# Performance work log

Hardware: AMD Instinct MI355X
Metric: run time of the kernel (lower is better)

Reference implementation:

```python
import jax, jax.numpy as jnp
import numpy as np

N, E, F_IN = 50000, 1_600_000, 256
HID, HEADS, NCLS = 8, 8, 16  # conv1: 8 heads x 8 dims (concat=64); conv2: 1 head -> 16 classes


def setup_inputs() -> dict:
    key = jax.random.key(0)
    ks = jax.random.split(key, 11)
    x = jax.random.normal(ks[0], (N, F_IN), dtype=jnp.float32)
    edge_index = jax.random.randint(ks[1], (2, E), 0, N, dtype=jnp.int32)
    s1 = 1.0 / np.sqrt(F_IN)
    W1 = jax.random.normal(ks[2], (F_IN, HEADS * HID), jnp.float32) * s1
    a_src1 = jax.random.normal(ks[3], (HEADS, HID), jnp.float32) * 0.1
    a_dst1 = jax.random.normal(ks[4], (HEADS, HID), jnp.float32) * 0.1
    b1 = jnp.zeros((HEADS * HID,), jnp.float32)
    s2 = 1.0 / np.sqrt(HEADS * HID)
    W2 = jax.random.normal(ks[5], (HEADS * HID, NCLS), jnp.float32) * s2
    a_src2 = jax.random.normal(ks[6], (1, NCLS), jnp.float32) * 0.1
    a_dst2 = jax.random.normal(ks[7], (1, NCLS), jnp.float32) * 0.1
    b2 = jnp.zeros((NCLS,), jnp.float32)
    return {"x": x, "edge_index": edge_index, "W1": W1, "a_src1": a_src1,
            "a_dst1": a_dst1, "b1": b1, "W2": W2, "a_src2": a_src2,
            "a_dst2": a_dst2, "b2": b2}


def _gat_conv(x, W, a_src, a_dst, bias, src, dst, n, heads, ch, concat):
    # per-head linear transform: [n, heads, ch]
    h = (x @ W).reshape(n, heads, ch)
    # additive attention logits per node, per head
    al_s = jnp.einsum('nhc,hc->nh', h, a_src)
    al_d = jnp.einsum('nhc,hc->nh', h, a_dst)
    e = jax.nn.leaky_relu(al_s[src] + al_d[dst], 0.2)  # [E_tot, heads]
    # segment softmax grouped by destination node (self-loops guarantee non-empty segments)
    m = jax.ops.segment_max(e, dst, num_segments=n)
    ex = jnp.exp(e - m[dst])
    den = jax.ops.segment_sum(ex, dst, num_segments=n)
    alpha = ex / den[dst]  # [E_tot, heads]
    # scatter-aggregate weighted neighbor features
    out = jax.ops.segment_sum(h[src] * alpha[:, :, None], dst, num_segments=n)
    out = out.reshape(n, heads * ch) if concat else out.mean(axis=1)
    return out + bias


def reference(x, edge_index, W1, a_src1, a_dst1, b1, W2, a_src2, a_dst2, b2):
    # add self-loops (PyG GATConv default)
    loops = jnp.arange(N, dtype=edge_index.dtype)
    src = jnp.concatenate([edge_index[0], loops])
    dst = jnp.concatenate([edge_index[1], loops])
    h = _gat_conv(x, W1, a_src1, a_dst1, b1, src, dst, N, HEADS, HID, True)
    h = jax.nn.elu(h)
    out = _gat_conv(h, W2, a_src2, a_dst2, b2, src, dst, N, 1, NCLS, False)
    return jax.nn.log_softmax(out, axis=1)
```

## Files before the change

### kernel.cpp

```cpp
#include <hip/hip_runtime.h>
#include <hip/hip_fp16.h>

#define NN   50000
#define FIN  256
#define C1   64
#define NH   8
#define NC   16
#define NE   1600000
#define NTOT (NE + NN)

#define CH   256
#define EPC  ((NTOT + CH - 1) / CH)
#define NCB  392
#define GB1  ((NN + 63) / 64)

typedef _Float16 half8 __attribute__((ext_vector_type(8)));
typedef _Float16 half4 __attribute__((ext_vector_type(4)));
typedef float f32x4 __attribute__((ext_vector_type(4)));

#define OFF_H1H   0
#define OFF_G1H   1600000
#define OFF_STAGE 3200000
#define OFF_H2H   3200000
#define OFF_ALS2  3600000
#define OFF_ALD2  3650000
#define OFF_ALS1  6400000
#define OFF_ALD1  6800000
#define OFF_HM    7200000
#define OFF_BASEK 7300352
#define OFF_BBASE 7400704
#define OFF_OFFS  7401600
#define OFF_SRC   7451700
#define OFF_W1T   9101700

__global__ __launch_bounds__(256) void k_wcvt(const float* __restrict__ W1,
                                              _Float16* __restrict__ w1t) {
    int t = blockIdx.x * 256 + threadIdx.x;
    int c = t >> 8, k = t & 255;
    w1t[t] = (_Float16)W1[k * C1 + c];
}

__global__ __launch_bounds__(256) void k_g1rh(const float* __restrict__ x,
                                              const _Float16* __restrict__ w1t,
                                              const float* __restrict__ as1,
                                              const float* __restrict__ ad1,
                                              __half* __restrict__ h1h,
                                              float* __restrict__ als,
                                              float* __restrict__ ald,
                                              const int* __restrict__ ei,
                                              int* __restrict__ H) {
    __shared__ _Float16 wsT[64][264];
    __shared__ _Float16 xs[64][40];
    const int tid = threadIdx.x;

    if (blockIdx.x >= GB1) {
        int* lh = (int*)xs;
        int k = blockIdx.x - GB1;
        for (int i = tid; i < NCB; i += 256) lh[i] = 0;
        __syncthreads();
        int e0 = k * EPC, e1 = min(e0 + EPC, NTOT);
        for (int e = e0 + tid; e < e1; e += 256) {
            int d = (e < NE) ? ei[NE + e] : (e - NE);
            atomicAdd(&lh[d >> 7], 1);
        }
        __syncthreads();
        for (int i = tid; i < NCB; i += 256) H[k * NCB + i] = lh[i];
        return;
    }

    const int r0 = blockIdx.x * 64;
    #pragma unroll
    for (int j = 0; j < 8; ++j) {
        int idx = tid * 8 + j * 2048;
        int c = idx >> 8, ko = idx & 255;
        *(half8*)(&wsT[c][ko]) = *(const half8*)(&w1t[idx]);
    }

    const int lane = tid & 63;
    const int wv   = tid >> 6;
    const int colb = lane & 15;
    const int rgrp = lane >> 4;
    f32x4 acc[4] = {};
    const int srow = tid >> 2;
    const int sq   = tid & 3;
    for (int k0 = 0; k0 < FIN; k0 += 32) {
        __syncthreads();
        {
            int grow = r0 + srow;
            float4 v0 = make_float4(0.f,0.f,0.f,0.f), v1 = v0;
            if (grow < NN) {
                const float4* xp = (const float4*)(&x[(size_t)grow * FIN + k0 + sq * 8]);
                v0 = xp[0]; v1 = xp[1];
            }
            half8 hv;
            hv[0]=(_Float16)v0.x; hv[1]=(_Float16)v0.y; hv[2]=(_Float16)v0.z; hv[3]=(_Float16)v0.w;
            hv[4]=(_Float16)v1.x; hv[5]=(_Float16)v1.y; hv[6]=(_Float16)v1.z; hv[7]=(_Float16)v1.w;
            *(half8*)(&xs[srow][sq * 8]) = hv;
        }
        __syncthreads();
        half8 a = *(half8*)(&xs[wv * 16 + colb][rgrp * 8]);
        #pragma unroll
        for (int ct = 0; ct < 4; ++ct) {
            half8 b = *(half8*)(&wsT[ct * 16 + colb][k0 + rgrp * 8]);
            acc[ct] = __builtin_amdgcn_mfma_f32_16x16x32_f16(a, b, acc[ct], 0, 0, 0);
        }
    }

    float a_s[4], a_d[4];
    #pragma unroll
    for (int ct = 0; ct < 4; ++ct) { a_s[ct] = as1[ct * 16 + colb]; a_d[ct] = ad1[ct * 16 + colb]; }
    #pragma unroll
    for (int j = 0; j < 4; ++j) {
        int row = r0 + wv * 16 + rgrp * 4 + j;
        bool rv = row < NN;
        #pragma unroll
        for (int ct = 0; ct < 4; ++ct) {
            if (rv) h1h[(size_t)row * C1 + ct * 16 + colb] = __float2half(acc[ct][j]);
            float p = acc[ct][j] * a_s[ct];
            p += __shfl_xor(p, 1); p += __shfl_xor(p, 2); p += __shfl_xor(p, 4);
            float q = acc[ct][j] * a_d[ct];
            q += __shfl_xor(q, 1); q += __shfl_xor(q, 2); q += __shfl_xor(q, 4);
            if (rv && (lane & 7) == 0) {
                int head = ct * 2 + (colb >> 3);
                als[row * NH + head] = p;
                ald[row * NH + head] = q;
            }
        }
    }
}

__global__ __launch_bounds__(256) void k_rsA(const int* __restrict__ H,
                                             int* __restrict__ basek,
                                             int* __restrict__ btot) {
    __shared__ int sc[CH];
    int b = blockIdx.x, t = threadIdx.x;
    int v = H[t * NCB + b];
    sc[t] = v;
    __syncthreads();
    for (int s = 1; s < CH; s <<= 1) {
        int u = (t >= s) ? sc[t - s] : 0;
        __syncthreads();
        sc[t] += u;
        __syncthreads();
    }
    basek[b * CH + t] = sc[t] - v;
    if (t == CH - 1) btot[b] = sc[t];
}

__global__ __launch_bounds__(512) void k_rsB(const int* __restrict__ btot,
                                             int* __restrict__ bbase,
                                             int* __restrict__ offs) {
    __shared__ int sc[512];
    int t = threadIdx.x;
    int v = (t < NCB) ? btot[t] : 0;
    sc[t] = v;
    __syncthreads();
    for (int s = 1; s < 512; s <<= 1) {
        int u = (t >= s) ? sc[t - s] : 0;
        __syncthreads();
        sc[t] += u;
        __syncthreads();
    }
    if (t < NCB) bbase[t] = sc[t] - v;
    if (t == NCB - 1) bbase[NCB] = sc[t];
    if (t == 0) offs[NN] = NTOT;
}

__global__ __launch_bounds__(256) void k_rscatter(const int* __restrict__ ei,
                                                  const int* __restrict__ basek,
                                                  const int* __restrict__ bbase,
                                                  int* __restrict__ stage) {
    __shared__ int lcur[NCB];
    int k = blockIdx.x;
    for (int i = threadIdx.x; i < NCB; i += 256)
        lcur[i] = bbase[i] + basek[i * CH + k];
    __syncthreads();
    int e0 = k * EPC, e1 = min(e0 + EPC, NTOT);
    for (int e = e0 + threadIdx.x; e < e1; e += 256) {
        int s, d;
        if (e < NE) { s = ei[e]; d = ei[NE + e]; }
        else        { s = e - NE; d = s; }
        int pos = atomicAdd(&lcur[d >> 7], 1);
        stage[pos] = (s << 7) | (d & 127);
    }
}

__global__ __launch_bounds__(256) void k_fsort(const int* __restrict__ stage,
                                               const int* __restrict__ bbase,
                                               int* __restrict__ offs,
                                               int* __restrict__ ssrc) {
    __shared__ int lc[128];
    __shared__ int ls[128];
    __shared__ int lcur[128];
    int b = blockIdx.x, t = threadIdx.x;
    int base = bbase[b];
    int n = bbase[b + 1] - base;
    if (t < 128) lc[t] = 0;
    __syncthreads();
    const int* sp = &stage[base];
    for (int i = t; i < n; i += 256) atomicAdd(&lc[sp[i] & 127], 1);
    __syncthreads();
    int v = (t < 128) ? lc[t] : 0;
    if (t < 128) ls[t] = v;
    __syncthreads();
    for (int s = 1; s < 128; s <<= 1) {
        int u = (t >= s && t < 128) ? ls[t - s] : 0;
        __syncthreads();
        if (t < 128) ls[t] += u;
        __syncthreads();
    }
    if (t < 128) {
        int excl = ls[t] - v;
        int d = b * 128 + t;
        if (d < NN) offs[d] = base + excl;
        lcur[t] = base + excl;
    }
    __syncthreads();
    for (int i = t; i < n; i += 256) {
        int u = sp[i];
        int pos = atomicAdd(&lcur[u & 127], 1);
        ssrc[pos] = u >> 7;
    }
}

__global__ __launch_bounds__(256) void k_agg1(const int* __restrict__ offs,
                                              const int* __restrict__ src,
                                              const __half* __restrict__ h1h,
                                              const float* __restrict__ als,
                                              const float* __restrict__ ald,
                                              const float* __restrict__ b1,
                                              _Float16* __restrict__ g1h) {
    int d = blockIdx.x * 4 + (threadIdx.x >> 6);
    if (d >= NN) return;
    const int l  = threadIdx.x & 63;
    const int q  = l >> 4, lc = l & 15;
    const int hg = lc >> 1;
    const int sub = l >> 3, hw = l & 7;
    const int lane_a = (q << 3) | hg;
    const int lane_b = lane_a + 32;
    const unsigned coff = (unsigned)lc * 8u;
    const unsigned hoff = (unsigned)hw * 4u;
    const char* h1b = (const char*)h1h;
    const char* alb = (const char*)als;
    int beg = offs[d], end = offs[d + 1];
    float aldv = ald[d * NH + hw];
    f32x4 acc = {0.f, 0.f, 0.f, 0.f};
    float wsum = 0.f;

    int r = beg;
    int e0 = r + sub, e1 = e0 + 8;
    int s0 = src[e0 < end ? e0 : end - 1];
    int s1 = src[e1 < end ? e1 : end - 1];
    while (r < end) {
        bool v0 = (r + sub) < end, v1 = (r + 8 + sub) < end;
        float lg0 = *(const float*)(alb + ((unsigned)s0 * 32u + hoff)) + aldv;
        float lg1 = *(const float*)(alb + ((unsigned)s1 * 32u + hoff)) + aldv;
        lg0 = lg0 > 0.f ? lg0 : 0.2f * lg0;
        lg1 = lg1 > 0.f ? lg1 : 0.2f * lg1;
        float w0 = v0 ? __expf(lg0) : 0.f;
        float w1 = v1 ? __expf(lg1) : 0.f;
        wsum += w0 + w1;
        int rn = r + 16;
        int s0n = s0, s1n = s1;
        if (rn < end) {
            int f0 = rn + sub, f1 = f0 + 8;
            s0n = src[f0 < end ? f0 : end - 1];
            s1n = src[f1 < end ? f1 : end - 1];
        }
        #pragma unroll
        for (int i = 0; i < 4; ++i) {
            int srcl = (i & 1) ? lane_b : lane_a;
            int sv   = __shfl((i < 2) ? s0 : s1, srcl);
            float wv = __shfl((i < 2) ? w0 : w1, srcl);
            half4 hv = *(const half4*)(h1b + ((unsigned)sv * 128u + coff));
            acc[0] += wv * (float)hv[0];
            acc[1] += wv * (float)hv[1];
            acc[2] += wv * (float)hv[2];
            acc[3] += wv * (float)hv[3];
        }
        s0 = s0n; s1 = s1n; r = rn;
    }
    #pragma unroll
    for (int k = 0; k < 4; ++k) {
        acc[k] += __shfl_xor(acc[k], 16);
        acc[k] += __shfl_xor(acc[k], 32);
    }
    wsum += __shfl_xor(wsum, 8);
    wsum += __shfl_xor(wsum, 16);
    wsum += __shfl_xor(wsum, 32);
    float den = __shfl(wsum, hg);
    if (q == 0) {
        half4 gv;
        #pragma unroll
        for (int k = 0; k < 4; ++k) {
            float o = acc[k] / den + b1[4 * lc + k];
            o = o > 0.f ? o : (__expf(o) - 1.f);
            gv[k] = (_Float16)o;
        }
        *(half4*)(&g1h[(size_t)d * C1 + 4 * lc]) = gv;
    }
}

__global__ __launch_bounds__(256) void k_gemm2(const _Float16* __restrict__ g1h,
                                               const float* __restrict__ W2,
                                               const float* __restrict__ as2,
                                               const float* __restrict__ ad2,
                                               _Float16* __restrict__ h2h,
                                               float* __restrict__ als2,
                                               float* __restrict__ ald2) {
    __shared__ float w2s[C1][17];
    __shared__ _Float16 hact[16][C1 + 8];
    int tid = threadIdx.x;
    for (int i = tid; i < C1 * NC; i += 256) w2s[i >> 4][i & 15] = W2[i];
    int ln = tid >> 4, j = tid & 15;
    int n = blockIdx.x * 16 + ln;
    if (n < NN)
        *(half4*)(&hact[ln][j * 4]) = *(const half4*)(&g1h[(size_t)n * C1 + j * 4]);
    __syncthreads();
    if (n >= NN) return;
    float sum = 0.f;
    #pragma unroll
    for (int c = 0; c < C1; ++c) sum += (float)hact[ln][c] * w2s[c][j];
    h2h[(size_t)n * NC + j] = (_Float16)sum;
    float ps = sum * as2[j], pd = sum * ad2[j];
    #pragma unroll
    for (int w = 1; w < 16; w <<= 1) {
        ps += __shfl_xor(ps, w);
        pd += __shfl_xor(pd, w);
    }
    if (j == 0) { als2[n] = ps; ald2[n] = pd; }
}

__global__ __launch_bounds__(256) void k_agg2(const int* __restrict__ offs,
                                              const int* __restrict__ src,
                                              const _Float16* __restrict__ h2h,
                                              const float* __restrict__ als2,
                                              const float* __restrict__ ald2,
                                              const float* __restrict__ b2,
                                              float* __restrict__ out) {
    int d = blockIdx.x * 16 + (threadIdx.x >> 4);
    if (d >= NN) return;
    int c = threadIdx.x & 15;
    const unsigned coff = (unsigned)c * 2u;
    const char* h2b = (const char*)h2h;
    const char* alb = (const char*)als2;
    int beg = offs[d], end = offs[d + 1];
    float aldv = ald2[d];
    float acc = 0.f, den = 0.f;
    for (int r = beg; r < end; r += 8) {
        int ss[8];
        float ww[8];
        #pragma unroll
        for (int i = 0; i < 8; ++i) {
            int e = r + i;
            ss[i] = src[e < end ? e : end - 1];
        }
        #pragma unroll
        for (int i = 0; i < 8; ++i) {
            float lg = *(const float*)(alb + (unsigned)ss[i] * 4u) + aldv;
            lg = lg > 0.f ? lg : 0.2f * lg;
            ww[i] = (r + i) < end ? __expf(lg) : 0.f;
        }
        #pragma unroll
        for (int i = 0; i < 8; ++i) {
            float hv = (float)*(const _Float16*)(h2b + ((unsigned)ss[i] * 32u + coff));
            acc += ww[i] * hv;
            den += ww[i];
        }
    }
    float o = acc / den + b2[c];
    float m = o;
    #pragma unroll
    for (int w = 1; w < 16; w <<= 1) m = fmaxf(m, __shfl_xor(m, w));
    float ex = __expf(o - m);
    float sm = ex;
    #pragma unroll
    for (int w = 1; w < 16; w <<= 1) sm += __shfl_xor(sm, w);
    out[(size_t)d * NC + c] = o - m - __logf(sm);
}

extern "C" void kernel_launch(void* const* d_in, const int* in_sizes, int n_in,
                              void* d_out, int out_size, void* d_ws, size_t ws_size,
                              hipStream_t stream) {
    const float* x   = (const float*)d_in[0];
    const int*   ei  = (const int*)  d_in[1];
    const float* W1  = (const float*)d_in[2];
    const float* as1 = (const float*)d_in[3];
    const float* ad1 = (const float*)d_in[4];
    const float* b1  = (const float*)d_in[5];
    const float* W2  = (const float*)d_in[6];
    const float* as2 = (const float*)d_in[7];
    const float* ad2 = (const float*)d_in[8];
    const float* b2  = (const float*)d_in[9];
    float* ws  = (float*)d_ws;
    float* out = (float*)d_out;

    __half*    h1h  = (__half*)(ws + OFF_H1H);
    _Float16*  g1h  = (_Float16*)(ws + OFF_G1H);
    _Float16*  h2h  = (_Float16*)(ws + OFF_H2H);
    _Float16*  w1t  = (_Float16*)(ws + OFF_W1T);
    float* als1 = ws + OFF_ALS1;
    float* ald1 = ws + OFF_ALD1;
    float* als2 = ws + OFF_ALS2;
    float* ald2 = ws + OFF_ALD2;
    int* H      = (int*)(ws + OFF_HM);
    int* basek  = (int*)(ws + OFF_BASEK);
    int* bbase  = (int*)(ws + OFF_BBASE);
    int* btot   = (int*)(ws + OFF_BBASE) + 400;
    int* offs   = (int*)(ws + OFF_OFFS);
    int* ssrc   = (int*)(ws + OFF_SRC);
    int* stage  = (int*)(ws + OFF_STAGE);

    k_wcvt    <<<64,             256, 0, stream>>>(W1, w1t);
    k_g1rh    <<<GB1 + CH,       256, 0, stream>>>(x, w1t, as1, ad1, h1h, als1, ald1, ei, H);
    k_rsA     <<<NCB,            256, 0, stream>>>(H, basek, btot);
    k_rsB     <<<1,              512, 0, stream>>>(btot, bbase, offs);
    k_rscatter<<<CH,             256, 0, stream>>>(ei, basek, bbase, stage);
    k_fsort   <<<NCB,            256, 0, stream>>>(stage, bbase, offs, ssrc);
    k_agg1    <<<(NN + 3) / 4,   256, 0, stream>>>(offs, ssrc, h1h, als1, ald1, b1, g1h);
    k_gemm2   <<<(NN + 15) / 16, 256, 0, stream>>>(g1h, W2, as2, ad2, h2h, als2, ald2);
    k_agg2    <<<(NN + 15) / 16, 256, 0, stream>>>(offs, ssrc, h2h, als2, ald2, b2, out);
}
```

Before: 137.8 us.

## Load GEMM1 A-fragments directly, stage output via LDS, software-pipeline agg1 logits

The first GEMM kernel no longer stages x tiles through shared memory. Each lane loads its own fp32 A fragment directly and converts it to fp16, which removes the per-k-step barriers. The results are then staged in LDS, which allows coalesced half8 stores of h1 and a per-thread dot product for the attention logits in place of shuffle reductions. The agg1 loop now computes the next chunk's attention weights after the feature gathers, overlapping the logit loads and exps with the accumulation. The trade-off is uncoalesced direct global loads of x and a small change in logit precision, since the logits are now computed from fp16-rounded h values.

```diff
diff --git a/kernel.cpp b/kernel.cpp
--- a/kernel.cpp
+++ b/kernel.cpp
@@ -44,17 +44,16 @@
                                               const _Float16* __restrict__ w1t,
                                               const float* __restrict__ as1,
                                               const float* __restrict__ ad1,
-                                              __half* __restrict__ h1h,
+                                              _Float16* __restrict__ h1h,
                                               float* __restrict__ als,
                                               float* __restrict__ ald,
                                               const int* __restrict__ ei,
                                               int* __restrict__ H) {
     __shared__ _Float16 wsT[64][264];
-    __shared__ _Float16 xs[64][40];
+    __shared__ int lh[NCB];
     const int tid = threadIdx.x;
 
     if (blockIdx.x >= GB1) {
-        int* lh = (int*)xs;
         int k = blockIdx.x - GB1;
         for (int i = tid; i < NCB; i += 256) lh[i] = 0;
         __syncthreads();
@@ -75,56 +74,62 @@
         int c = idx >> 8, ko = idx & 255;
         *(half8*)(&wsT[c][ko]) = *(const half8*)(&w1t[idx]);
     }
+    __syncthreads();
 
     const int lane = tid & 63;
     const int wv   = tid >> 6;
     const int colb = lane & 15;
     const int rgrp = lane >> 4;
+    const int arow = r0 + wv * 16 + colb;
+    const bool arv = arow < NN;
     f32x4 acc[4] = {};
-    const int srow = tid >> 2;
-    const int sq   = tid & 3;
-    for (int k0 = 0; k0 < FIN; k0 += 32) {
-        __syncthreads();
-        {
-            int grow = r0 + srow;
-            float4 v0 = make_float4(0.f,0.f,0.f,0.f), v1 = v0;
-            if (grow < NN) {
-                const float4* xp = (const float4*)(&x[(size_t)grow * FIN + k0 + sq * 8]);
-                v0 = xp[0]; v1 = xp[1];
+    #pragma unroll
+    for (int s = 0; s < 8; ++s) {
+        float4 v0 = make_float4(0.f,0.f,0.f,0.f), v1 = v0;
+        if (arv) {
+            const float4* xp = (const float4*)(&x[(size_t)arow * FIN + s * 32 + rgrp * 8]);
+            v0 = xp[0]; v1 = xp[1];
+        }
+        half8 a;
+        a[0]=(_Float16)v0.x; a[1]=(_Float16)v0.y; a[2]=(_Float16)v0.z; a[3]=(_Float16)v0.w;
+        a[4]=(_Float16)v1.x; a[5]=(_Float16)v1.y; a[6]=(_Float16)v1.z; a[7]=(_Float16)v1.w;
+        #pragma unroll
+        for (int ct = 0; ct < 4; ++ct) {
+            half8 b = *(half8*)(&wsT[ct * 16 + colb][s * 32 + rgrp * 8]);
+            acc[ct] = __builtin_amdgcn_mfma_f32_16x16x32_f16(a, b, acc[ct], 0, 0, 0);
+        }
+    }
+    __syncthreads();
+    _Float16 (*hstore)[72] = (_Float16(*)[72])wsT;
+    #pragma unroll
+    for (int j = 0; j < 4; ++j) {
+        int row = wv * 16 + rgrp * 4 + j;
+        #pragma unroll
+        for (int ct = 0; ct < 4; ++ct)
+            hstore[row][ct * 16 + colb] = (_Float16)acc[ct][j];
+    }
+    __syncthreads();
+    {
+        int row = tid >> 2, seg = tid & 3;
+        int grow = r0 + row;
+        if (grow < NN) {
+            half8 h0 = *(half8*)(&hstore[row][seg * 16]);
+            half8 h1v = *(half8*)(&hstore[row][seg * 16 + 8]);
+            *(half8*)(&h1h[(size_t)grow * C1 + seg * 16])     = h0;
+            *(half8*)(&h1h[(size_t)grow * C1 + seg * 16 + 8]) = h1v;
+            float ps0 = 0.f, pd0 = 0.f, ps1 = 0.f, pd1 = 0.f;
+            #pragma unroll
+            for (int u = 0; u < 8; ++u) {
+                float a0 = (float)h0[u], a1 = (float)h1v[u];
+                ps0 += a0 * as1[seg * 16 + u];
+                pd0 += a0 * ad1[seg * 16 + u];
+                ps1 += a1 * as1[seg * 16 + 8 + u];
+                pd1 += a1 * ad1[seg * 16 + 8 + u];
             }
-            half8 hv;
-            hv[0]=(_Float16)v0.x; hv[1]=(_Float16)v0.y; hv[2]=(_Float16)v0.z; hv[3]=(_Float16)v0.w;
-            hv[4]=(_Float16)v1.x; hv[5]=(_Float16)v1.y; hv[6]=(_Float16)v1.z; hv[7]=(_Float16)v1.w;
-            *(half8*)(&xs[srow][sq * 8]) = hv;
-        }
-        __syncthreads();
-        half8 a = *(half8*)(&xs[wv * 16 + colb][rgrp * 8]);
-        #pragma unroll
-        for (int ct = 0; ct < 4; ++ct) {
-            half8 b = *(half8*)(&wsT[ct * 16 + colb][k0 + rgrp * 8]);
-            acc[ct] = __builtin_amdgcn_mfma_f32_16x16x32_f16(a, b, acc[ct], 0, 0, 0);
-        }
-    }
-
-    float a_s[4], a_d[4];
-    #pragma unroll
-    for (int ct = 0; ct < 4; ++ct) { a_s[ct] = as1[ct * 16 + colb]; a_d[ct] = ad1[ct * 16 + colb]; }
-    #pragma unroll
-    for (int j = 0; j < 4; ++j) {
-        int row = r0 + wv * 16 + rgrp * 4 + j;
-        bool rv = row < NN;
-        #pragma unroll
-        for (int ct = 0; ct < 4; ++ct) {
-            if (rv) h1h[(size_t)row * C1 + ct * 16 + colb] = __float2half(acc[ct][j]);
-            float p = acc[ct][j] * a_s[ct];
-            p += __shfl_xor(p, 1); p += __shfl_xor(p, 2); p += __shfl_xor(p, 4);
-            float q = acc[ct][j] * a_d[ct];
-            q += __shfl_xor(q, 1); q += __shfl_xor(q, 2); q += __shfl_xor(q, 4);
-            if (rv && (lane & 7) == 0) {
-                int head = ct * 2 + (colb >> 3);
-                als[row * NH + head] = p;
-                ald[row * NH + head] = q;
-            }
+            als[grow * NH + seg * 2]     = ps0;
+            als[grow * NH + seg * 2 + 1] = ps1;
+            ald[grow * NH + seg * 2]     = pd0;
+            ald[grow * NH + seg * 2 + 1] = pd1;
         }
     }
 }
@@ -251,34 +256,47 @@
     int e0 = r + sub, e1 = e0 + 8;
     int s0 = src[e0 < end ? e0 : end - 1];
     int s1 = src[e1 < end ? e1 : end - 1];
-    while (r < end) {
-        bool v0 = (r + sub) < end, v1 = (r + 8 + sub) < end;
+    {
         float lg0 = *(const float*)(alb + ((unsigned)s0 * 32u + hoff)) + aldv;
         float lg1 = *(const float*)(alb + ((unsigned)s1 * 32u + hoff)) + aldv;
         lg0 = lg0 > 0.f ? lg0 : 0.2f * lg0;
         lg1 = lg1 > 0.f ? lg1 : 0.2f * lg1;
-        float w0 = v0 ? __expf(lg0) : 0.f;
-        float w1 = v1 ? __expf(lg1) : 0.f;
-        wsum += w0 + w1;
-        int rn = r + 16;
-        int s0n = s0, s1n = s1;
-        if (rn < end) {
-            int f0 = rn + sub, f1 = f0 + 8;
-            s0n = src[f0 < end ? f0 : end - 1];
-            s1n = src[f1 < end ? f1 : end - 1];
-        }
-        #pragma unroll
-        for (int i = 0; i < 4; ++i) {
-            int srcl = (i & 1) ? lane_b : lane_a;
-            int sv   = __shfl((i < 2) ? s0 : s1, srcl);
-            float wv = __shfl((i < 2) ? w0 : w1, srcl);
-            half4 hv = *(const half4*)(h1b + ((unsigned)sv * 128u + coff));
-            acc[0] += wv * (float)hv[0];
-            acc[1] += wv * (float)hv[1];
-            acc[2] += wv * (float)hv[2];
-            acc[3] += wv * (float)hv[3];
-        }
-        s0 = s0n; s1 = s1n; r = rn;
+        s0 = e0 < end ? s0 : s0;
+        float w0t = e0 < end ? __expf(lg0) : 0.f;
+        float w1t = e1 < end ? __expf(lg1) : 0.f;
+        acc[0] = acc[0];
+        float w0 = w0t, w1 = w1t;
+        while (r < end) {
+            int rn = r + 16;
+            bool more = rn < end;
+            int s0n = s0, s1n = s1;
+            if (more) {
+                int f0 = rn + sub, f1 = f0 + 8;
+                s0n = src[f0 < end ? f0 : end - 1];
+                s1n = src[f1 < end ? f1 : end - 1];
+            }
+            wsum += w0 + w1;
+            #pragma unroll
+            for (int i = 0; i < 4; ++i) {
+                int srcl = (i & 1) ? lane_b : lane_a;
+                int sv   = __shfl((i < 2) ? s0 : s1, srcl);
+                float wv = __shfl((i < 2) ? w0 : w1, srcl);
+                half4 hv = *(const half4*)(h1b + ((unsigned)sv * 128u + coff));
+                acc[0] += wv * (float)hv[0];
+                acc[1] += wv * (float)hv[1];
+                acc[2] += wv * (float)hv[2];
+                acc[3] += wv * (float)hv[3];
+            }
+            if (more) {
+                float g0 = *(const float*)(alb + ((unsigned)s0n * 32u + hoff)) + aldv;
+                float g1 = *(const float*)(alb + ((unsigned)s1n * 32u + hoff)) + aldv;
+                g0 = g0 > 0.f ? g0 : 0.2f * g0;
+                g1 = g1 > 0.f ? g1 : 0.2f * g1;
+                w0 = (rn + sub) < end ? __expf(g0) : 0.f;
+                w1 = (rn + 8 + sub) < end ? __expf(g1) : 0.f;
+            }
+            s0 = s0n; s1 = s1n; r = rn;
+        }
     }
     #pragma unroll
     for (int k = 0; k < 4; ++k) {
@@ -395,7 +413,7 @@
     float* ws  = (float*)d_ws;
     float* out = (float*)d_out;
 
-    __half*    h1h  = (__half*)(ws + OFF_H1H);
+    _Float16*  h1h  = (_Float16*)(ws + OFF_H1H);
     _Float16*  g1h  = (_Float16*)(ws + OFF_G1H);
     _Float16*  h2h  = (_Float16*)(ws + OFF_H2H);
     _Float16*  w1t  = (_Float16*)(ws + OFF_W1T);
@@ -417,7 +435,7 @@
     k_rsB     <<<1,              512, 0, stream>>>(btot, bbase, offs);
     k_rscatter<<<CH,             256, 0, stream>>>(ei, basek, bbase, stage);
     k_fsort   <<<NCB,            256, 0, stream>>>(stage, bbase, offs, ssrc);
-    k_agg1    <<<(NN + 3) / 4,   256, 0, stream>>>(offs, ssrc, h1h, als1, ald1, b1, g1h);
+    k_agg1    <<<(NN + 3) / 4,   256, 0, stream>>>(offs, ssrc, (const __half*)h1h, als1, ald1, b1, g1h);
     k_gemm2   <<<(NN + 15) / 16, 256, 0, stream>>>(g1h, W2, as2, ad2, h2h, als2, ald2);
     k_agg2    <<<(NN + 15) / 16, 256, 0, stream>>>(offs, ssrc, h2h, als2, ald2, b2, out);
 }
```

New measurement: 137.4 us. No clear change (-0.3%).
